# Optimization experiments

Measured on AMD Instinct MI355X. Metric: run time of the kernel, lower is better.

The kernel has to match this reference:

```python
import jax, jax.numpy as jnp
import numpy as np

N, E = 40000, 640000
EMB, HID, H, TXT = 128, 128, 4, 384
C = HID // H  # per-head channels = 32


def _prelu(x, a):
    return jnp.where(x >= 0, x, a * x)


def _layernorm(x, g, b, eps=1e-5):
    m = jnp.mean(x, axis=-1, keepdims=True)
    v = jnp.mean((x - m) ** 2, axis=-1, keepdims=True)
    return (x - m) / jnp.sqrt(v + eps) * g + b


def _gat_conv(h, src, dst, W, att_src, att_dst, bias):
    # PyG GATConv (concat=True, eval mode): lin has no bias, self-loops already in src/dst.
    xh = (h @ W.T).reshape(N, H, C)                      # [N,H,C]
    a_src = jnp.sum(xh * att_src, axis=-1)               # [N,H]
    a_dst = jnp.sum(xh * att_dst, axis=-1)               # [N,H]
    alpha = jax.nn.leaky_relu(a_src[src] + a_dst[dst], negative_slope=0.2)  # [Et,H]
    amax = jax.ops.segment_max(alpha, dst, num_segments=N)
    ex = jnp.exp(alpha - amax[dst])
    denom = jax.ops.segment_sum(ex, dst, num_segments=N)
    coef = ex / denom[dst]                               # scatter-softmax over dst
    out = jax.ops.segment_sum(xh[src] * coef[:, :, None], dst, num_segments=N)
    return out.reshape(N, H * C) + bias


def setup_inputs() -> dict:
    key = jax.random.key(0)
    ks = jax.random.split(key, 20)
    nrm = lambda k, s, sc=0.05: jax.random.normal(k, s, jnp.float32) * sc
    inp = {
        "x": nrm(ks[0], (N, EMB), 1.0),
        "num_x": nrm(ks[1], (N, 1), 1.0),
        "num_mask": jnp.ones((N,), jnp.float32),
        "txt_x": nrm(ks[2], (N, TXT), 1.0),
        "txt_mask": jnp.ones((N,), jnp.float32),
        "edge_index": jax.random.randint(ks[3], (2, E), 0, N, jnp.int32),
        "num_proj_w": nrm(ks[4], (EMB, 1)), "num_proj_b": jnp.zeros((EMB,), jnp.float32),
        "txt_proj_w": nrm(ks[5], (EMB, TXT)), "txt_proj_b": jnp.zeros((EMB,), jnp.float32),
        "node_proj_w": nrm(ks[6], (HID, EMB)), "node_proj_b": jnp.zeros((HID,), jnp.float32),
        "prelu0_a": jnp.full((HID,), 0.25, jnp.float32),
        "conv1_w": nrm(ks[7], (HID, HID)), "att_src1": nrm(ks[8], (H, C)), "att_dst1": nrm(ks[9], (H, C)), "bias1": jnp.zeros((HID,), jnp.float32),
        "norm1_g": jnp.ones((HID,), jnp.float32), "norm1_b": jnp.zeros((HID,), jnp.float32),
        "prelu1_a": jnp.full((HID,), 0.25, jnp.float32),
        "conv2_w": nrm(ks[10], (HID, HID)), "att_src2": nrm(ks[11], (H, C)), "att_dst2": nrm(ks[12], (H, C)), "bias2": jnp.zeros((HID,), jnp.float32),
        "norm2_g": jnp.ones((HID,), jnp.float32), "norm2_b": jnp.zeros((HID,), jnp.float32),
        "prelu2_a": jnp.full((HID,), 0.25, jnp.float32),
        "out_w": nrm(ks[13], (1, HID)), "out_b": jnp.zeros((1,), jnp.float32),
    }
    return inp


def reference(x, num_x, num_mask, txt_x, txt_mask, edge_index,
              num_proj_w, num_proj_b, txt_proj_w, txt_proj_b,
              node_proj_w, node_proj_b, prelu0_a,
              conv1_w, att_src1, att_dst1, bias1, norm1_g, norm1_b, prelu1_a,
              conv2_w, att_src2, att_dst2, bias2, norm2_g, norm2_b, prelu2_a,
              out_w, out_b):
    # add self loops (PyG GATConv default)
    loop = jnp.arange(N, dtype=edge_index.dtype)
    src = jnp.concatenate([edge_index[0], loop])
    dst = jnp.concatenate([edge_index[1], loop])

    h = (num_x * num_mask[:, None]) @ num_proj_w.T + num_proj_b
    h = h + (txt_x * txt_mask[:, None]) @ txt_proj_w.T + txt_proj_b
    h = h + x @ node_proj_w.T + node_proj_b
    h = _prelu(h, prelu0_a)

    h = _gat_conv(h, src, dst, conv1_w, att_src1, att_dst1, bias1)
    h = _prelu(_layernorm(h, norm1_g, norm1_b), prelu1_a)  # dropout: eval mode -> identity

    h = _gat_conv(h, src, dst, conv2_w, att_src2, att_dst2, bias2)
    h = _prelu(_layernorm(h, norm2_g, norm2_b), prelu2_a)

    return (h @ out_w.T + out_b).squeeze(-1)  # [N]
```

## Files before the change

kernel.cpp:

```cpp
#include <hip/hip_runtime.h>
#include <stdint.h>

typedef unsigned short u16;
typedef unsigned int u32;
typedef __attribute__((ext_vector_type(8))) short bf16x8;
typedef __attribute__((ext_vector_type(4))) float f32x4;

__device__ __forceinline__ float bf2f(u32 u) {
    union { u32 i; float f; } v; v.i = u << 16; return v.f;
}
__device__ __forceinline__ u16 f2bf(float f) {
    u32 x = __float_as_uint(f);
    return (u16)((x + 0x7fffu + ((x >> 16) & 1u)) >> 16);
}
__device__ __forceinline__ float wred_sum(float v) {
#pragma unroll
    for (int o = 32; o > 0; o >>= 1) v += __shfl_xor(v, o, 64);
    return v;
}
__device__ __forceinline__ bf16x8 cvt8(float4 a, float4 b) {
    union { uint4 u; bf16x8 v; } t;
    t.u.x = (u32)f2bf(a.x) | ((u32)f2bf(a.y) << 16);
    t.u.y = (u32)f2bf(a.z) | ((u32)f2bf(a.w) << 16);
    t.u.z = (u32)f2bf(b.x) | ((u32)f2bf(b.y) << 16);
    t.u.w = (u32)f2bf(b.z) | ((u32)f2bf(b.w) << 16);
    return t.v;
}
__device__ __forceinline__ bf16x8 ld16B(const u16* p, size_t off) {
    union { uint4 u; bf16x8 b; } t; t.u = *(const uint4*)(p + off); return t.b;
}
__device__ __forceinline__ void glds16(const void* g, void* l) {
    __builtin_amdgcn_global_load_lds(
        (const __attribute__((address_space(1))) void*)g,
        (__attribute__((address_space(3))) void*)l, 16, 0, 0);
}
__device__ __forceinline__ void stageW_glds(const u16* __restrict__ W, int ldk, int koff,
                                            u16* swl, int tid) {
    int w64 = tid >> 6;
#pragma unroll
    for (int it = 0; it < 8; ++it) {
        int row = it * 16 + (tid >> 4);
        int sphys = tid & 15;
        int ssrc = sphys ^ (row & 7);
        const u16* g = W + (size_t)row * ldk + koff + ssrc * 8;
        u16* dst = swl + (size_t)(it * 256 + w64 * 64) * 8;
        glds16(g, dst);
    }
}
__device__ __forceinline__ bf16x8 ldBx(const u16* swl, int ct, int ks, int l16, int quad) {
    int row = ct * 16 + l16;
    int slot = (ks * 4 + quad) ^ (row & 7);
    union { uint4 u; bf16x8 b; } t;
    t.u = *(const uint4*)&swl[row * 128 + slot * 8];
    return t.b;
}

__global__ void k_cvtw(const float* __restrict__ s0, const float* __restrict__ s1,
                       const float* __restrict__ s2, const float* __restrict__ s3,
                       u16* __restrict__ d, int n0, int n1, int n2, int n3) {
    int i = (blockIdx.x * 256 + threadIdx.x) * 8;
    int t = i;
    const float* s;
    if (t < n0) s = s0 + t;
    else if ((t -= n0) < n1) s = s1 + t;
    else if ((t -= n1) < n2) s = s2 + t;
    else if ((t -= n2) < n3) s = s3 + t;
    else return;
    float4 a = *(const float4*)s, b = *(const float4*)(s + 4);
    uint4 v;
    v.x = (u32)f2bf(a.x) | ((u32)f2bf(a.y) << 16);
    v.y = (u32)f2bf(a.z) | ((u32)f2bf(a.w) << 16);
    v.z = (u32)f2bf(b.x) | ((u32)f2bf(b.y) << 16);
    v.w = (u32)f2bf(b.z) | ((u32)f2bf(b.w) << 16);
    *(uint4*)(d + i) = v;
}

__global__ void k_zero(int* __restrict__ p, int n) {
    int i = blockIdx.x * 256 + threadIdx.x;
    if (i < n) p[i] = 0;
}
__global__ void k_hist(const int* __restrict__ dst, int E, int* __restrict__ deg) {
    int e = blockIdx.x * 256 + threadIdx.x;
    if (e < E) atomicAdd(&deg[dst[e]], 1);
}
__global__ __launch_bounds__(1024) void k_scanA(const int* __restrict__ deg, int n,
                                                int* __restrict__ out, int* __restrict__ bsum) {
    __shared__ int wsum[16];
    int t = threadIdx.x, w = t >> 6, lane = t & 63;
    int i0 = blockIdx.x * 4096 + t * 4;
    int4 v = make_int4(0, 0, 0, 0);
    if (i0 + 3 < n) v = *(const int4*)&deg[i0];
    else {
        if (i0 < n)     v.x = deg[i0];
        if (i0 + 1 < n) v.y = deg[i0 + 1];
        if (i0 + 2 < n) v.z = deg[i0 + 2];
    }
    int tsum = v.x + v.y + v.z + v.w;
    int s = tsum;
#pragma unroll
    for (int o = 1; o < 64; o <<= 1) { int u = __shfl_up(s, o, 64); if (lane >= o) s += u; }
    if (lane == 63) wsum[w] = s;
    __syncthreads();
    if (w == 0 && lane < 16) {
        int ws = wsum[lane];
#pragma unroll
        for (int o = 1; o < 16; o <<= 1) { int u = __shfl_up(ws, o, 64); if (lane >= o) ws += u; }
        wsum[lane] = ws;
    }
    __syncthreads();
    int woff = (w == 0) ? 0 : wsum[w - 1];
    int p = woff + s - tsum;
    if (i0 + 3 < n) {
        int4 o4; o4.x = p; o4.y = p + v.x; o4.z = p + v.x + v.y; o4.w = p + v.x + v.y + v.z;
        *(int4*)&out[i0] = o4;
    } else {
        int pp = p;
        if (i0 < n)     { out[i0] = pp;     pp += v.x; }
        if (i0 + 1 < n) { out[i0 + 1] = pp; pp += v.y; }
        if (i0 + 2 < n) { out[i0 + 2] = pp; }
    }
    if (t == 0) bsum[blockIdx.x] = wsum[15];
}
__global__ void k_scanB(int* __restrict__ bsum, int nb, int* __restrict__ total) {
    int lane = threadIdx.x;
    int v = (lane < nb) ? bsum[lane] : 0;
    int s = v;
#pragma unroll
    for (int o = 1; o < 64; o <<= 1) { int u = __shfl_up(s, o, 64); if (lane >= o) s += u; }
    if (lane < nb) bsum[lane] = s - v;
    if (lane == 63) total[0] = s;
}
__global__ void k_scanC(int* __restrict__ rowptr, int* __restrict__ cursor,
                        const int* __restrict__ boff, int n) {
    int i = blockIdx.x * 256 + threadIdx.x;
    if (i < n) {
        int r = rowptr[i] + boff[i >> 12];
        rowptr[i] = r; cursor[i] = r;
    }
}
__global__ void k_scatter(const int* __restrict__ srcp, const int* __restrict__ dstp, int E,
                          int* __restrict__ cursor, int* __restrict__ col) {
    int e = blockIdx.x * 256 + threadIdx.x;
    if (e < E) {
        int p = atomicAdd(&cursor[dstp[e]], 1);
        col[p] = srcp[e];
    }
}

__global__ __launch_bounds__(256) void k_fused1(
    const float* __restrict__ x, const float* __restrict__ numx, const float* __restrict__ numm,
    const float* __restrict__ txt, const float* __restrict__ txtm,
    const float* __restrict__ numw, const float* __restrict__ numb,
    const float* __restrict__ txtb, const float* __restrict__ nodeb,
    const float* __restrict__ pa,
    const u16* __restrict__ txtwb, const u16* __restrict__ nodewb, const u16* __restrict__ w1b,
    const float* __restrict__ atts, const float* __restrict__ attd,
    u16* __restrict__ xh, float* __restrict__ asrc, float* __restrict__ adst) {
    __shared__ u16 swl[2][128 * 128];
    int tid = threadIdx.x, w = tid >> 6, lane = tid & 63, quad = lane >> 4, l16 = lane & 15;
    int nb = blockIdx.x * 64 + w * 16;

    const float* trow = txt + (size_t)(nb + l16) * 384 + quad * 8;
    const float* xrow = x + (size_t)(nb + l16) * 128 + quad * 8;

    f32x4 acc[8];
#pragma unroll
    for (int ct = 0; ct < 8; ++ct) { f32x4 z = {0.f, 0.f, 0.f, 0.f}; acc[ct] = z; }

#define LDA(P, base)                                                            \
    float4 P##0 = *(const float4*)((base) + 0),  P##1 = *(const float4*)((base) + 4);   \
    float4 P##2 = *(const float4*)((base) + 32), P##3 = *(const float4*)((base) + 36);  \
    float4 P##4 = *(const float4*)((base) + 64), P##5 = *(const float4*)((base) + 68);  \
    float4 P##6 = *(const float4*)((base) + 96), P##7 = *(const float4*)((base) + 100);

#define COMPUTE(buf, P)                                                         \
    {                                                                           \
        bf16x8 f0_ = cvt8(P##0, P##1), f1_ = cvt8(P##2, P##3);                  \
        bf16x8 f2_ = cvt8(P##4, P##5), f3_ = cvt8(P##6, P##7);                  \
        _Pragma("unroll")                                                       \
        for (int ct = 0; ct < 8; ++ct)                                          \
            acc[ct] = __builtin_amdgcn_mfma_f32_16x16x32_bf16(                  \
                f0_, ldBx(buf, ct, 0, l16, quad), acc[ct], 0, 0, 0);            \
        _Pragma("unroll")                                                       \
        for (int ct = 0; ct < 8; ++ct)                                          \
            acc[ct] = __builtin_amdgcn_mfma_f32_16x16x32_bf16(                  \
                f1_, ldBx(buf, ct, 1, l16, quad), acc[ct], 0, 0, 0);            \
        _Pragma("unroll")                                                       \
        for (int ct = 0; ct < 8; ++ct)                                          \
            acc[ct] = __builtin_amdgcn_mfma_f32_16x16x32_bf16(                  \
                f2_, ldBx(buf, ct, 2, l16, quad), acc[ct], 0, 0, 0);            \
        _Pragma("unroll")                                                       \
        for (int ct = 0; ct < 8; ++ct)                                          \
            acc[ct] = __builtin_amdgcn_mfma_f32_16x16x32_bf16(                  \
                f3_, ldBx(buf, ct, 3, l16, quad), acc[ct], 0, 0, 0);            \
    }

    stageW_glds(txtwb, 384, 0, swl[0], tid);
    LDA(Aa, trow)
    __syncthreads();

    stageW_glds(txtwb, 384, 128, swl[1], tid);
    LDA(Ab, trow + 128)
    COMPUTE(swl[0], Aa)
    __syncthreads();

    stageW_glds(txtwb, 384, 256, swl[0], tid);
    LDA(Ac, trow + 256)
    COMPUTE(swl[1], Ab)
    __syncthreads();

    stageW_glds(nodewb, 128, 0, swl[1], tid);
    LDA(Ad, xrow)
    COMPUTE(swl[0], Ac)
#pragma unroll
    for (int r = 0; r < 4; ++r) {
        float tm = txtm[nb + quad * 4 + r];
#pragma unroll
        for (int ct = 0; ct < 8; ++ct) acc[ct][r] *= tm;
    }
    __syncthreads();

    stageW_glds(w1b, 128, 0, swl[0], tid);
    COMPUTE(swl[1], Ad)
    {
        float nm[4];
#pragma unroll
        for (int r = 0; r < 4; ++r) {
            int n = nb + quad * 4 + r;
            nm[r] = numx[n] * numm[n];
        }
#pragma unroll
        for (int ct = 0; ct < 8; ++ct) {
            int c = ct * 16 + l16;
            float cw = numw[c];
            float cb = numb[c] + txtb[c] + nodeb[c];
            float pav = pa[c];
#pragma unroll
            for (int r = 0; r < 4; ++r) {
                float v = acc[ct][r] + nm[r] * cw + cb;
                acc[ct][r] = v >= 0.f ? v : pav * v;
            }
        }
    }
    __syncthreads();

    u16* shw = ((u16*)swl[1]) + w * 16 * 136;
#pragma unroll
    for (int ct = 0; ct < 8; ++ct) {
        int c = ct * 16 + l16;
#pragma unroll
        for (int r = 0; r < 4; ++r)
            shw[(quad * 4 + r) * 136 + c] = f2bf(acc[ct][r]);
    }
    f32x4 a2[8];
#pragma unroll
    for (int ct = 0; ct < 8; ++ct) { f32x4 z = {0.f, 0.f, 0.f, 0.f}; a2[ct] = z; }
#pragma unroll
    for (int ks = 0; ks < 4; ++ks) {
        bf16x8 a0 = ld16B(shw, l16 * 136 + ks * 32 + quad * 8);
#pragma unroll
        for (int ct = 0; ct < 8; ++ct)
            a2[ct] = __builtin_amdgcn_mfma_f32_16x16x32_bf16(
                a0, ldBx(swl[0], ct, ks, l16, quad), a2[ct], 0, 0, 0);
    }
#undef LDA
#undef COMPUTE

#pragma unroll
    for (int ct = 0; ct < 8; ++ct) {
        int c = ct * 16 + l16;
#pragma unroll
        for (int r = 0; r < 4; ++r)
            xh[(size_t)(nb + quad * 4 + r) * 128 + c] = f2bf(a2[ct][r]);
    }
    float as_[8], ad_[8];
#pragma unroll
    for (int ct = 0; ct < 8; ++ct) {
        int c = ct * 16 + l16;
        as_[ct] = atts[c];
        ad_[ct] = attd[c];
    }
#pragma unroll
    for (int hh = 0; hh < 4; ++hh) {
        float vs[4], vd[4];
#pragma unroll
        for (int r = 0; r < 4; ++r) {
            vs[r] = a2[2 * hh][r] * as_[2 * hh] + a2[2 * hh + 1][r] * as_[2 * hh + 1];
            vd[r] = a2[2 * hh][r] * ad_[2 * hh] + a2[2 * hh + 1][r] * ad_[2 * hh + 1];
        }
#pragma unroll
        for (int o = 1; o <= 8; o <<= 1) {
#pragma unroll
            for (int r = 0; r < 4; ++r) {
                vs[r] += __shfl_xor(vs[r], o, 64);
                vd[r] += __shfl_xor(vd[r], o, 64);
            }
        }
        if ((l16 >> 2) == hh) {
            int r = l16 & 3;
            float ss = (r == 0) ? vs[0] : (r == 1) ? vs[1] : (r == 2) ? vs[2] : vs[3];
            float dd = (r == 0) ? vd[0] : (r == 1) ? vd[1] : (r == 2) ? vd[2] : vd[3];
            int n = nb + quad * 4 + r;
            asrc[n * 4 + hh] = ss;
            adst[n * 4 + hh] = dd;
        }
    }
}

__global__ __launch_bounds__(256) void k_xh(
    const u16* __restrict__ h, const u16* __restrict__ Wb,
    const float* __restrict__ att_s, const float* __restrict__ att_d,
    u16* __restrict__ xh, float* __restrict__ asrc, float* __restrict__ adst) {
    __shared__ u16 swl[128 * 128];
    int tid = threadIdx.x;
    int w = tid >> 6, lane = tid & 63, quad = lane >> 4, l16 = lane & 15;
    int nb = blockIdx.x * 64 + w * 16;

    stageW_glds(Wb, 128, 0, swl, tid);
    const u16* hrow = h + (size_t)(nb + l16) * 128 + quad * 8;
    uint4 A0 = *(const uint4*)(hrow);
    uint4 A1 = *(const uint4*)(hrow + 32);
    uint4 A2 = *(const uint4*)(hrow + 64);
    uint4 A3 = *(const uint4*)(hrow + 96);
    f32x4 acc[8];
#pragma unroll
    for (int ct = 0; ct < 8; ++ct) { f32x4 z = {0.f, 0.f, 0.f, 0.f}; acc[ct] = z; }
    __syncthreads();
    union { uint4 u; bf16x8 b; } t0, t1, t2, t3;
    t0.u = A0; t1.u = A1; t2.u = A2; t3.u = A3;
#pragma unroll
    for (int ct = 0; ct < 8; ++ct)
        acc[ct] = __builtin_amdgcn_mfma_f32_16x16x32_bf16(
            t0.b, ldBx(swl, ct, 0, l16, quad), acc[ct], 0, 0, 0);
#pragma unroll
    for (int ct = 0; ct < 8; ++ct)
        acc[ct] = __builtin_amdgcn_mfma_f32_16x16x32_bf16(
            t1.b, ldBx(swl, ct, 1, l16, quad), acc[ct], 0, 0, 0);
#pragma unroll
    for (int ct = 0; ct < 8; ++ct)
        acc[ct] = __builtin_amdgcn_mfma_f32_16x16x32_bf16(
            t2.b, ldBx(swl, ct, 2, l16, quad), acc[ct], 0, 0, 0);
#pragma unroll
    for (int ct = 0; ct < 8; ++ct)
        acc[ct] = __builtin_amdgcn_mfma_f32_16x16x32_bf16(
            t3.b, ldBx(swl, ct, 3, l16, quad), acc[ct], 0, 0, 0);
#pragma unroll
    for (int ct = 0; ct < 8; ++ct) {
        int c = ct * 16 + l16;
#pragma unroll
        for (int r = 0; r < 4; ++r) {
            int n = nb + quad * 4 + r;
            xh[(size_t)n * 128 + c] = f2bf(acc[ct][r]);
        }
    }
    float as_[8], ad_[8];
#pragma unroll
    for (int ct = 0; ct < 8; ++ct) {
        int c = ct * 16 + l16;
        as_[ct] = att_s[c];
        ad_[ct] = att_d[c];
    }
#pragma unroll
    for (int hh = 0; hh < 4; ++hh) {
        float vs[4], vd[4];
#pragma unroll
        for (int r = 0; r < 4; ++r) {
            vs[r] = acc[2 * hh][r] * as_[2 * hh] + acc[2 * hh + 1][r] * as_[2 * hh + 1];
            vd[r] = acc[2 * hh][r] * ad_[2 * hh] + acc[2 * hh + 1][r] * ad_[2 * hh + 1];
        }
#pragma unroll
        for (int o = 1; o <= 8; o <<= 1) {
#pragma unroll
            for (int r = 0; r < 4; ++r) {
                vs[r] += __shfl_xor(vs[r], o, 64);
                vd[r] += __shfl_xor(vd[r], o, 64);
            }
        }
        if ((l16 >> 2) == hh) {
            int r = l16 & 3;
            float ss = (r == 0) ? vs[0] : (r == 1) ? vs[1] : (r == 2) ? vs[2] : vs[3];
            float dd = (r == 0) ? vd[0] : (r == 1) ? vd[1] : (r == 2) ? vd[2] : vd[3];
            int n = nb + quad * 4 + r;
            asrc[n * 4 + hh] = ss;
            adst[n * 4 + hh] = dd;
        }
    }
}

__global__ __launch_bounds__(64) void k_agg(
    const u16* __restrict__ xh, const float* __restrict__ asrc, const float* __restrict__ adst,
    const int* __restrict__ rowptr, const int* __restrict__ col,
    const float* __restrict__ bias, const float* __restrict__ g, const float* __restrict__ b,
    const float* __restrict__ pa, u16* __restrict__ hnext,
    const float* __restrict__ outw, const float* __restrict__ outb, float* __restrict__ outy,
    int is_final) {
    __shared__ int   scol[64];
    __shared__ float scoef[64][4];
    int n = blockIdx.x, lane = threadIdx.x;
    int beg = rowptr[n], end = rowptr[n + 1];
    const float4* asrc4 = (const float4*)asrc;

    float4 adv = ((const float4*)adst)[n];
    float ad[4] = { adv.x, adv.y, adv.z, adv.w };
    float4 asv = asrc4[n];
    float els[4];
#pragma unroll
    for (int h = 0; h < 4; h++) {
        float a = ((const float*)&asv)[h] + ad[h];
        a = a >= 0.f ? a : 0.2f * a;
        els[h] = __expf(a);
    }
    int hh = lane >> 4;
    u32 vself = ((const u32*)(xh + (size_t)n * 128))[lane];
    float ac0[8], ac1[8];
#pragma unroll
    for (int q = 0; q < 8; ++q) { ac0[q] = 0.f; ac1[q] = 0.f; }
    ac0[0] = els[hh] * bf2f(vself & 0xffffu);
    ac1[0] = els[hh] * bf2f(vself >> 16);
    float l[4] = { 0.f, 0.f, 0.f, 0.f };

    for (int base = beg; base < end; base += 64) {
        int e = base + lane;
        int cnt = min(64, end - base);
        if (e < end) {
            int s = col[e];
            float4 av = asrc4[s];
            scol[lane] = s;
            float cf[4];
#pragma unroll
            for (int h = 0; h < 4; h++) {
                float a = ((const float*)&av)[h] + ad[h];
                a = a >= 0.f ? a : 0.2f * a;
                cf[h] = __expf(a);
                l[h] += cf[h];
            }
            *(float4*)scoef[lane] = make_float4(cf[0], cf[1], cf[2], cf[3]);
        }
        __syncthreads();
        int j = 0;
        for (; j + 7 < cnt; j += 8) {
            int ss[8]; float cc[8]; u32 vv[8];
#pragma unroll
            for (int q = 0; q < 8; ++q) { ss[q] = scol[j + q]; cc[q] = scoef[j + q][hh]; }
#pragma unroll
            for (int q = 0; q < 8; ++q) vv[q] = ((const u32*)(xh + (size_t)ss[q] * 128))[lane];
#pragma unroll
            for (int q = 0; q < 8; ++q) {
                ac0[q] += cc[q] * bf2f(vv[q] & 0xffffu);
                ac1[q] += cc[q] * bf2f(vv[q] >> 16);
            }
        }
        for (; j + 3 < cnt; j += 4) {
            int ss[4]; float cc[4]; u32 vv[4];
#pragma unroll
            for (int q = 0; q < 4; ++q) { ss[q] = scol[j + q]; cc[q] = scoef[j + q][hh]; }
#pragma unroll
            for (int q = 0; q < 4; ++q) vv[q] = ((const u32*)(xh + (size_t)ss[q] * 128))[lane];
#pragma unroll
            for (int q = 0; q < 4; ++q) {
                ac0[q] += cc[q] * bf2f(vv[q] & 0xffffu);
                ac1[q] += cc[q] * bf2f(vv[q] >> 16);
            }
        }
        for (; j < cnt; ++j) {
            int s0 = scol[j];
            float c0 = scoef[j][hh];
            u32 v0 = ((const u32*)(xh + (size_t)s0 * 128))[lane];
            ac0[0] += c0 * bf2f(v0 & 0xffffu);
            ac1[0] += c0 * bf2f(v0 >> 16);
        }
        __syncthreads();
    }
    float acc0 = 0.f, acc1 = 0.f;
#pragma unroll
    for (int q = 0; q < 8; ++q) { acc0 += ac0[q]; acc1 += ac1[q]; }

    float L[4];
#pragma unroll
    for (int h = 0; h < 4; h++) L[h] = wred_sum(l[h]) + els[h];
    float inv = 1.f / L[hh];
    acc0 *= inv;
    acc1 *= inv;

    int c0i = 2 * lane;
    float2 bi = *(const float2*)(bias + c0i);
    acc0 += bi.x; acc1 += bi.y;

    float mean = wred_sum(acc0 + acc1) * (1.f / 128.f);
    float d0 = acc0 - mean, d1 = acc1 - mean;
    float var = wred_sum(d0 * d0 + d1 * d1) * (1.f / 128.f);
    float rstd = rsqrtf(var + 1e-5f);
    float2 gg = *(const float2*)(g + c0i);
    float2 bb = *(const float2*)(b + c0i);
    float2 pp = *(const float2*)(pa + c0i);
    float y0 = d0 * rstd * gg.x + bb.x;
    float y1 = d1 * rstd * gg.y + bb.y;
    y0 = y0 >= 0.f ? y0 : pp.x * y0;
    y1 = y1 >= 0.f ? y1 : pp.y * y1;

    if (is_final) {
        float2 ow = *(const float2*)(outw + c0i);
        float dot = wred_sum(y0 * ow.x + y1 * ow.y);
        if (lane == 0) outy[n] = dot + outb[0];
    } else {
        ((u32*)(hnext + (size_t)n * 128))[lane] = (u32)f2bf(y0) | ((u32)f2bf(y1) << 16);
    }
}

extern "C" void kernel_launch(void* const* d_in, const int* in_sizes, int n_in,
                              void* d_out, int out_size, void* d_ws, size_t ws_size,
                              hipStream_t stream) {
    const int N = in_sizes[2];
    const int E = in_sizes[5] / 2;

    const float* x      = (const float*)d_in[0];
    const float* numx   = (const float*)d_in[1];
    const float* numm   = (const float*)d_in[2];
    const float* txt    = (const float*)d_in[3];
    const float* txtm   = (const float*)d_in[4];
    const int*   ei     = (const int*)d_in[5];
    const float* numw   = (const float*)d_in[6];
    const float* numb   = (const float*)d_in[7];
    const float* txtw   = (const float*)d_in[8];
    const float* txtb   = (const float*)d_in[9];
    const float* nodew  = (const float*)d_in[10];
    const float* nodeb  = (const float*)d_in[11];
    const float* pa0    = (const float*)d_in[12];
    const float* conv1w = (const float*)d_in[13];
    const float* atts1  = (const float*)d_in[14];
    const float* attd1  = (const float*)d_in[15];
    const float* bias1  = (const float*)d_in[16];
    const float* g1     = (const float*)d_in[17];
    const float* b1     = (const float*)d_in[18];
    const float* pa1    = (const float*)d_in[19];
    const float* conv2w = (const float*)d_in[20];
    const float* atts2  = (const float*)d_in[21];
    const float* attd2  = (const float*)d_in[22];
    const float* bias2  = (const float*)d_in[23];
    const float* g2     = (const float*)d_in[24];
    const float* b2     = (const float*)d_in[25];
    const float* pa2    = (const float*)d_in[26];
    const float* outw   = (const float*)d_in[27];
    const float* outb   = (const float*)d_in[28];

    const int* srcp = ei;
    const int* dstp = ei + E;

    const int szTxtw = in_sizes[8];
    const int szNode = in_sizes[10];
    const int szW1   = in_sizes[13];
    const int szW2   = in_sizes[20];
    const int szWAll = szTxtw + szNode + szW1 + szW2;

    char* p = (char*)d_ws;
    auto alloc = [&](size_t bytes) -> void* {
        void* q = (void*)p;
        p += (bytes + 255) & ~(size_t)255;
        return q;
    };
    u16*   hA     = (u16*)alloc((size_t)N * 128 * 2);
    u16*   hB     = (u16*)alloc((size_t)N * 128 * 2);
    float* asrc   = (float*)alloc((size_t)N * 4 * 4);
    float* adst   = (float*)alloc((size_t)N * 4 * 4);
    int*   deg    = (int*)alloc((size_t)N * 4);
    int*   rowptr = (int*)alloc((size_t)(N + 1) * 4);
    int*   cursor = (int*)alloc((size_t)N * 4);
    int*   col    = (int*)alloc((size_t)E * 4);
    int*   bsum   = (int*)alloc(64 * 4);
    u16*   wbf    = (u16*)alloc((size_t)szWAll * 2);

    u16* txtwb  = wbf;
    u16* nodewb = wbf + szTxtw;
    u16* w1b    = nodewb + szNode;
    u16* w2b    = w1b + szW1;

    k_cvtw<<<(szWAll / 8 + 255) / 256, 256, 0, stream>>>(
        txtw, nodew, conv1w, conv2w, wbf, szTxtw, szNode, szW1, szW2);

    const int nbScan = (N + 4095) / 4096;
    k_zero<<<(N + 255) / 256, 256, 0, stream>>>(deg, N);
    k_hist<<<(E + 255) / 256, 256, 0, stream>>>(dstp, E, deg);
    k_scanA<<<nbScan, 1024, 0, stream>>>(deg, N, rowptr, bsum);
    k_scanB<<<1, 64, 0, stream>>>(bsum, nbScan, rowptr + N);
    k_scanC<<<(N + 255) / 256, 256, 0, stream>>>(rowptr, cursor, bsum, N);
    k_scatter<<<(E + 255) / 256, 256, 0, stream>>>(srcp, dstp, E, cursor, col);

    const int gProj = N / 64;

    k_fused1<<<gProj, 256, 0, stream>>>(x, numx, numm, txt, txtm, numw, numb,
                                        txtb, nodeb, pa0,
                                        txtwb, nodewb, w1b, atts1, attd1, hB, asrc, adst);
    k_agg<<<N, 64, 0, stream>>>(hB, asrc, adst, rowptr, col, bias1, g1, b1, pa1,
                                hA, nullptr, nullptr, nullptr, 0);

    k_xh<<<gProj, 256, 0, stream>>>(hA, w2b, atts2, attd2, hB, asrc, adst);
    k_agg<<<N, 64, 0, stream>>>(hB, asrc, adst, rowptr, col, bias2, g2, b2, pa2,
                                nullptr, outw, outb, (float*)d_out, 1);
}
```

Before: 324.0 us.

## Load GEMM weight fragments directly from global memory instead of LDS staging

Removes the LDS staging of bf16 weight tiles (global_load_lds plus swizzled reads and block barriers) in both the fused projection kernel and the per-layer xh kernel. Each wave now reads its B fragments straight from global memory, relying on L1/L2 to serve the small weight matrices. This frees LDS and removes the barriers, which may raise occupancy. In exchange every wave issues redundant global loads of the same weights and can stall on their latency in front of the MFMAs.

```diff
diff --git a/kernel.cpp b/kernel.cpp
--- a/kernel.cpp
+++ b/kernel.cpp
@@ -29,30 +29,9 @@
 __device__ __forceinline__ bf16x8 ld16B(const u16* p, size_t off) {
     union { uint4 u; bf16x8 b; } t; t.u = *(const uint4*)(p + off); return t.b;
 }
-__device__ __forceinline__ void glds16(const void* g, void* l) {
-    __builtin_amdgcn_global_load_lds(
-        (const __attribute__((address_space(1))) void*)g,
-        (__attribute__((address_space(3))) void*)l, 16, 0, 0);
-}
-__device__ __forceinline__ void stageW_glds(const u16* __restrict__ W, int ldk, int koff,
-                                            u16* swl, int tid) {
-    int w64 = tid >> 6;
-#pragma unroll
-    for (int it = 0; it < 8; ++it) {
-        int row = it * 16 + (tid >> 4);
-        int sphys = tid & 15;
-        int ssrc = sphys ^ (row & 7);
-        const u16* g = W + (size_t)row * ldk + koff + ssrc * 8;
-        u16* dst = swl + (size_t)(it * 256 + w64 * 64) * 8;
-        glds16(g, dst);
-    }
-}
-__device__ __forceinline__ bf16x8 ldBx(const u16* swl, int ct, int ks, int l16, int quad) {
-    int row = ct * 16 + l16;
-    int slot = (ks * 4 + quad) ^ (row & 7);
-    union { uint4 u; bf16x8 b; } t;
-    t.u = *(const uint4*)&swl[row * 128 + slot * 8];
-    return t.b;
+__device__ __forceinline__ bf16x8 ldBg(const u16* __restrict__ W, int ldk, int koff,
+                                       int ks, int ct, int l16, int quad) {
+    return ld16B(W, (size_t)(ct * 16 + l16) * ldk + koff + ks * 32 + quad * 8);
 }
 
 __global__ void k_cvtw(const float* __restrict__ s0, const float* __restrict__ s1,
@@ -156,7 +135,7 @@
     const u16* __restrict__ txtwb, const u16* __restrict__ nodewb, const u16* __restrict__ w1b,
     const float* __restrict__ atts, const float* __restrict__ attd,
     u16* __restrict__ xh, float* __restrict__ asrc, float* __restrict__ adst) {
-    __shared__ u16 swl[2][128 * 128];
+    __shared__ u16 sh[4][16 * 136];
     int tid = threadIdx.x, w = tid >> 6, lane = tid & 63, quad = lane >> 4, l16 = lane & 15;
     int nb = blockIdx.x * 64 + w * 16;
 
@@ -167,90 +146,64 @@
 #pragma unroll
     for (int ct = 0; ct < 8; ++ct) { f32x4 z = {0.f, 0.f, 0.f, 0.f}; acc[ct] = z; }
 
-#define LDA(P, base)                                                            \
-    float4 P##0 = *(const float4*)((base) + 0),  P##1 = *(const float4*)((base) + 4);   \
-    float4 P##2 = *(const float4*)((base) + 32), P##3 = *(const float4*)((base) + 36);  \
-    float4 P##4 = *(const float4*)((base) + 64), P##5 = *(const float4*)((base) + 68);  \
-    float4 P##6 = *(const float4*)((base) + 96), P##7 = *(const float4*)((base) + 100);
-
-#define COMPUTE(buf, P)                                                         \
+#define CHUNKG(Wp, ldk, koff, Ap)                                               \
     {                                                                           \
-        bf16x8 f0_ = cvt8(P##0, P##1), f1_ = cvt8(P##2, P##3);                  \
-        bf16x8 f2_ = cvt8(P##4, P##5), f3_ = cvt8(P##6, P##7);                  \
+        const float* pA_ = (Ap);                                                \
+        float4 A0 = *(const float4*)(pA_ + 0),  A1 = *(const float4*)(pA_ + 4);   \
+        float4 A2 = *(const float4*)(pA_ + 32), A3 = *(const float4*)(pA_ + 36);  \
+        float4 A4 = *(const float4*)(pA_ + 64), A5 = *(const float4*)(pA_ + 68);  \
+        float4 A6 = *(const float4*)(pA_ + 96), A7 = *(const float4*)(pA_ + 100); \
+        bf16x8 f0_ = cvt8(A0, A1), f1_ = cvt8(A2, A3);                          \
+        bf16x8 f2_ = cvt8(A4, A5), f3_ = cvt8(A6, A7);                          \
         _Pragma("unroll")                                                       \
         for (int ct = 0; ct < 8; ++ct)                                          \
             acc[ct] = __builtin_amdgcn_mfma_f32_16x16x32_bf16(                  \
-                f0_, ldBx(buf, ct, 0, l16, quad), acc[ct], 0, 0, 0);            \
+                f0_, ldBg(Wp, ldk, koff, 0, ct, l16, quad), acc[ct], 0, 0, 0);  \
         _Pragma("unroll")                                                       \
         for (int ct = 0; ct < 8; ++ct)                                          \
             acc[ct] = __builtin_amdgcn_mfma_f32_16x16x32_bf16(                  \
-                f1_, ldBx(buf, ct, 1, l16, quad), acc[ct], 0, 0, 0);            \
+                f1_, ldBg(Wp, ldk, koff, 1, ct, l16, quad), acc[ct], 0, 0, 0);  \
         _Pragma("unroll")                                                       \
         for (int ct = 0; ct < 8; ++ct)                                          \
             acc[ct] = __builtin_amdgcn_mfma_f32_16x16x32_bf16(                  \
-                f2_, ldBx(buf, ct, 2, l16, quad), acc[ct], 0, 0, 0);            \
+                f2_, ldBg(Wp, ldk, koff, 2, ct, l16, quad), acc[ct], 0, 0, 0);  \
         _Pragma("unroll")                                                       \
         for (int ct = 0; ct < 8; ++ct)                                          \
             acc[ct] = __builtin_amdgcn_mfma_f32_16x16x32_bf16(                  \
-                f3_, ldBx(buf, ct, 3, l16, quad), acc[ct], 0, 0, 0);            \
-    }
-
-    stageW_glds(txtwb, 384, 0, swl[0], tid);
-    LDA(Aa, trow)
-    __syncthreads();
-
-    stageW_glds(txtwb, 384, 128, swl[1], tid);
-    LDA(Ab, trow + 128)
-    COMPUTE(swl[0], Aa)
-    __syncthreads();
-
-    stageW_glds(txtwb, 384, 256, swl[0], tid);
-    LDA(Ac, trow + 256)
-    COMPUTE(swl[1], Ab)
-    __syncthreads();
-
-    stageW_glds(nodewb, 128, 0, swl[1], tid);
-    LDA(Ad, xrow)
-    COMPUTE(swl[0], Ac)
+                f3_, ldBg(Wp, ldk, koff, 3, ct, l16, quad), acc[ct], 0, 0, 0);  \
+    }
+
+    CHUNKG(txtwb, 384, 0,   trow)
+    CHUNKG(txtwb, 384, 128, trow + 128)
+    CHUNKG(txtwb, 384, 256, trow + 256)
 #pragma unroll
     for (int r = 0; r < 4; ++r) {
         float tm = txtm[nb + quad * 4 + r];
 #pragma unroll
         for (int ct = 0; ct < 8; ++ct) acc[ct][r] *= tm;
     }
-    __syncthreads();
-
-    stageW_glds(w1b, 128, 0, swl[0], tid);
-    COMPUTE(swl[1], Ad)
-    {
-        float nm[4];
-#pragma unroll
-        for (int r = 0; r < 4; ++r) {
-            int n = nb + quad * 4 + r;
-            nm[r] = numx[n] * numm[n];
-        }
-#pragma unroll
-        for (int ct = 0; ct < 8; ++ct) {
-            int c = ct * 16 + l16;
-            float cw = numw[c];
-            float cb = numb[c] + txtb[c] + nodeb[c];
-            float pav = pa[c];
-#pragma unroll
-            for (int r = 0; r < 4; ++r) {
-                float v = acc[ct][r] + nm[r] * cw + cb;
-                acc[ct][r] = v >= 0.f ? v : pav * v;
-            }
-        }
-    }
-    __syncthreads();
-
-    u16* shw = ((u16*)swl[1]) + w * 16 * 136;
+    CHUNKG(nodewb, 128, 0, xrow)
+#undef CHUNKG
+
+    float nm[4];
+#pragma unroll
+    for (int r = 0; r < 4; ++r) {
+        int n = nb + quad * 4 + r;
+        nm[r] = numx[n] * numm[n];
+    }
+    u16* shw = sh[w];
 #pragma unroll
     for (int ct = 0; ct < 8; ++ct) {
         int c = ct * 16 + l16;
-#pragma unroll
-        for (int r = 0; r < 4; ++r)
-            shw[(quad * 4 + r) * 136 + c] = f2bf(acc[ct][r]);
+        float cw = numw[c];
+        float cb = numb[c] + txtb[c] + nodeb[c];
+        float pav = pa[c];
+#pragma unroll
+        for (int r = 0; r < 4; ++r) {
+            float v = acc[ct][r] + nm[r] * cw + cb;
+            v = v >= 0.f ? v : pav * v;
+            shw[(quad * 4 + r) * 136 + c] = f2bf(v);
+        }
     }
     f32x4 a2[8];
 #pragma unroll
@@ -261,11 +214,8 @@
 #pragma unroll
         for (int ct = 0; ct < 8; ++ct)
             a2[ct] = __builtin_amdgcn_mfma_f32_16x16x32_bf16(
-                a0, ldBx(swl[0], ct, ks, l16, quad), a2[ct], 0, 0, 0);
-    }
-#undef LDA
-#undef COMPUTE
-
+                a0, ldBg(w1b, 128, 0, ks, ct, l16, quad), a2[ct], 0, 0, 0);
+    }
 #pragma unroll
     for (int ct = 0; ct < 8; ++ct) {
         int c = ct * 16 + l16;
@@ -311,39 +261,34 @@
     const u16* __restrict__ h, const u16* __restrict__ Wb,
     const float* __restrict__ att_s, const float* __restrict__ att_d,
     u16* __restrict__ xh, float* __restrict__ asrc, float* __restrict__ adst) {
-    __shared__ u16 swl[128 * 128];
     int tid = threadIdx.x;
     int w = tid >> 6, lane = tid & 63, quad = lane >> 4, l16 = lane & 15;
     int nb = blockIdx.x * 64 + w * 16;
 
-    stageW_glds(Wb, 128, 0, swl, tid);
     const u16* hrow = h + (size_t)(nb + l16) * 128 + quad * 8;
-    uint4 A0 = *(const uint4*)(hrow);
-    uint4 A1 = *(const uint4*)(hrow + 32);
-    uint4 A2 = *(const uint4*)(hrow + 64);
-    uint4 A3 = *(const uint4*)(hrow + 96);
+    bf16x8 A0 = ld16B(hrow, 0);
+    bf16x8 A1 = ld16B(hrow, 32);
+    bf16x8 A2 = ld16B(hrow, 64);
+    bf16x8 A3 = ld16B(hrow, 96);
     f32x4 acc[8];
 #pragma unroll
     for (int ct = 0; ct < 8; ++ct) { f32x4 z = {0.f, 0.f, 0.f, 0.f}; acc[ct] = z; }
-    __syncthreads();
-    union { uint4 u; bf16x8 b; } t0, t1, t2, t3;
-    t0.u = A0; t1.u = A1; t2.u = A2; t3.u = A3;
 #pragma unroll
     for (int ct = 0; ct < 8; ++ct)
         acc[ct] = __builtin_amdgcn_mfma_f32_16x16x32_bf16(
-            t0.b, ldBx(swl, ct, 0, l16, quad), acc[ct], 0, 0, 0);
+            A0, ldBg(Wb, 128, 0, 0, ct, l16, quad), acc[ct], 0, 0, 0);
 #pragma unroll
     for (int ct = 0; ct < 8; ++ct)
         acc[ct] = __builtin_amdgcn_mfma_f32_16x16x32_bf16(
-            t1.b, ldBx(swl, ct, 1, l16, quad), acc[ct], 0, 0, 0);
+            A1, ldBg(Wb, 128, 0, 1, ct, l16, quad), acc[ct], 0, 0, 0);
 #pragma unroll
     for (int ct = 0; ct < 8; ++ct)
         acc[ct] = __builtin_amdgcn_mfma_f32_16x16x32_bf16(
-            t2.b, ldBx(swl, ct, 2, l16, quad), acc[ct], 0, 0, 0);
+            A2, ldBg(Wb, 128, 0, 2, ct, l16, quad), acc[ct], 0, 0, 0);
 #pragma unroll
     for (int ct = 0; ct < 8; ++ct)
         acc[ct] = __builtin_amdgcn_mfma_f32_16x16x32_bf16(
-            t3.b, ldBx(swl, ct, 3, l16, quad), acc[ct], 0, 0, 0);
+            A3, ldBg(Wb, 128, 0, 3, ct, l16, quad), acc[ct], 0, 0, 0);
 #pragma unroll
     for (int ct = 0; ct < 8; ++ct) {
         int c = ct * 16 + l16;
```

New measurement: 365.7 us. 1.13x slower.
